# Optimization experiments

Measured on AMD Instinct MI355X. Metric: run time of the kernel, lower is better.

## Reference

```python
import jax, jax.numpy as jnp
import numpy as np

B, L, D_IN, D_H, D_OUT = 8, 1024, 1024, 1024, 1024


def setup_inputs() -> dict:
    key = jax.random.key(0)
    ks = jax.random.split(key, 9)
    s = 0.02  # weight scale to keep ReLU chain stable
    return {
        "leaves": jax.random.normal(ks[0], (B, L, D_IN), dtype=jnp.float32),
        "V_w": jax.random.normal(ks[1], (D_H, D_IN), dtype=jnp.float32) * s,
        "V_b": jax.random.normal(ks[2], (D_H,), dtype=jnp.float32) * s,
        "U_w": jax.random.normal(ks[3], (D_H, D_H), dtype=jnp.float32) * s,
        "U_b": jax.random.normal(ks[4], (D_H,), dtype=jnp.float32) * s,
        "W_w": jax.random.normal(ks[5], (D_H, D_H), dtype=jnp.float32) * s,
        "W_b": jax.random.normal(ks[6], (D_H,), dtype=jnp.float32) * s,
        "O_w": jax.random.normal(ks[7], (D_OUT, D_H), dtype=jnp.float32) * s,
        "O_b": jax.random.normal(ks[8], (D_OUT,), dtype=jnp.float32) * s,
    }


def reference(leaves, V_w, V_b, U_w, U_b, W_w, W_b, O_w, O_b):
    # Leaf encoding: h_leaf = relu(V(x))            [B, L, H]
    h = jax.nn.relu(jnp.einsum("bli,hi->blh", leaves, V_w) + V_b)
    # Depth-batched recursion over the complete binary tree:
    # combined = relu(U(left) + W(right)); log2(L) levels, node count halves.
    while h.shape[1] > 1:
        left, right = h[:, 0::2], h[:, 1::2]  # [B, n/2, H] each
        h = jax.nn.relu(
            jnp.einsum("bnh,gh->bng", left, U_w) + U_b
            + jnp.einsum("bnh,gh->bng", right, W_w) + W_b
        )
    root = h[:, 0]  # [B, H]
    logits = jnp.einsum("bh,oh->bo", root, O_w) + O_b
    return jax.nn.log_softmax(logits, axis=-1)
```

## Files before the change

### kernel.cpp

```cpp
#include <hip/hip_runtime.h>
#include <hip/hip_bf16.h>
#include <math.h>

typedef __bf16 bf16_t;
typedef __bf16 bf16x8 __attribute__((ext_vector_type(8)));
typedef __bf16 bf16x4 __attribute__((ext_vector_type(4)));
typedef float  f32x4  __attribute__((ext_vector_type(4)));

#define GLD_LDS16(g, l)                                                          \
  __builtin_amdgcn_global_load_lds((const __attribute__((address_space(1))) void*)(g), \
                                   (__attribute__((address_space(3))) void*)(l), 16, 0, 0)

__global__ __launch_bounds__(256) void k_cvt_all(const float* __restrict__ leaves,
                                                 const float* __restrict__ V_w,
                                                 const float* __restrict__ O_w,
                                                 const float* __restrict__ U_w,
                                                 const float* __restrict__ W_w,
                                                 const float* __restrict__ U_b,
                                                 const float* __restrict__ W_b,
                                                 bf16_t* __restrict__ leaves_bf,
                                                 bf16_t* __restrict__ Vw_bf,
                                                 bf16_t* __restrict__ Ow_bf,
                                                 bf16_t* __restrict__ UW_bf,
                                                 float* __restrict__ buw) {
  const int gtid = blockIdx.x * 256 + threadIdx.x;
  const int G = gridDim.x * 256;
  for (int i = gtid; i < 2097152; i += G) {
    float4 v = reinterpret_cast<const float4*>(leaves)[i];
    bf16x4 o; o[0] = (bf16_t)v.x; o[1] = (bf16_t)v.y; o[2] = (bf16_t)v.z; o[3] = (bf16_t)v.w;
    reinterpret_cast<bf16x4*>(leaves_bf)[i] = o;
  }
  for (int i = gtid; i < 262144; i += G) {
    float4 v = reinterpret_cast<const float4*>(V_w)[i];
    bf16x4 o; o[0] = (bf16_t)v.x; o[1] = (bf16_t)v.y; o[2] = (bf16_t)v.z; o[3] = (bf16_t)v.w;
    reinterpret_cast<bf16x4*>(Vw_bf)[i] = o;
  }
  for (int i = gtid; i < 262144; i += G) {
    float4 v = reinterpret_cast<const float4*>(O_w)[i];
    bf16x4 o; o[0] = (bf16_t)v.x; o[1] = (bf16_t)v.y; o[2] = (bf16_t)v.z; o[3] = (bf16_t)v.w;
    reinterpret_cast<bf16x4*>(Ow_bf)[i] = o;
  }
  for (int idx = gtid; idx < 524288; idx += G) {
    int i = idx * 4;
    int g = i >> 11;
    int k = i & 2047;
    const float* src = (k < 1024) ? (U_w + g * 1024 + k) : (W_w + g * 1024 + (k - 1024));
    float4 v = *reinterpret_cast<const float4*>(src);
    bf16x4 o; o[0] = (bf16_t)v.x; o[1] = (bf16_t)v.y; o[2] = (bf16_t)v.z; o[3] = (bf16_t)v.w;
    reinterpret_cast<bf16x4*>(UW_bf)[idx] = o;
  }
  if (gtid < 1024) buw[gtid] = U_b[gtid] + W_b[gtid];
}

template <int TM, int TN, bool SPLIT>
__global__ __launch_bounds__(256, (TM == 128 ? 3 : 4)) void k_gemm(
    const bf16_t* __restrict__ A, const bf16_t* __restrict__ Bw,
    const float* __restrict__ bias, bf16_t* __restrict__ C,
    float* __restrict__ P, int M, int Kstride, int kchunk) {
  constexpr int MI = TM / 32;
  constexpr int NJ = TN / 32;
  constexpr int VM = TM / 64 + TN / 64;
  __shared__ bf16_t As[3][TM * 32];
  __shared__ bf16_t Bs[3][TN * 32];

  const int tid = threadIdx.x;
  const int lane = tid & 63;
  const int wave = tid >> 6;
  const int wr = wave >> 1, wc = wave & 1;
  const int bm = blockIdx.x, bn = blockIdx.y, bz = blockIdx.z;

  const bf16_t* Abase = A + (size_t)bm * TM * Kstride + (size_t)bz * kchunk;
  const bf16_t* Bbase = Bw + (size_t)bn * TN * Kstride + (size_t)bz * kchunk;

  f32x4 acc[MI][NJ] = {};
  const int rl = lane & 15, kq = lane >> 4;

  auto stage = [&](int buf, int ko) {
#pragma unroll
    for (int it = 0; it < TM / 64; ++it) {
      int c = tid + 256 * it;
      int r = c >> 2, kbp = c & 3;
      int kb = kbp ^ ((r >> 1) & 3);
      GLD_LDS16(Abase + (size_t)r * Kstride + ko + kb * 8, &As[buf][c * 8]);
    }
#pragma unroll
    for (int it = 0; it < TN / 64; ++it) {
      int c = tid + 256 * it;
      int r = c >> 2, kbp = c & 3;
      int kb = kbp ^ ((r >> 1) & 3);
      GLD_LDS16(Bbase + (size_t)r * Kstride + ko + kb * 8, &Bs[buf][c * 8]);
    }
  };

  const int kiters = kchunk >> 5;
  stage(0, 0);
  stage(1, 32);

  int cur = 0;
  for (int t = 0; t < kiters; ++t) {
    if (t + 1 < kiters) asm volatile("s_waitcnt vmcnt(%0)" :: "i"(VM) : "memory");
    else                asm volatile("s_waitcnt vmcnt(0)" ::: "memory");
    __builtin_amdgcn_s_barrier();
    __builtin_amdgcn_sched_barrier(0);
    if (t + 2 < kiters) {
      int b2 = cur + 2; if (b2 >= 3) b2 -= 3;
      stage(b2, (t + 2) * 32);
    }
    bf16x8 af[MI], bfr[NJ];
#pragma unroll
    for (int i = 0; i < MI; ++i) {
      int r = wr * (TM / 2) + i * 16 + rl;
      int kbp = kq ^ ((r >> 1) & 3);
      af[i] = *reinterpret_cast<const bf16x8*>(&As[cur][r * 32 + kbp * 8]);
    }
#pragma unroll
    for (int j = 0; j < NJ; ++j) {
      int r = wc * (TN / 2) + j * 16 + rl;
      int kbp = kq ^ ((r >> 1) & 3);
      bfr[j] = *reinterpret_cast<const bf16x8*>(&Bs[cur][r * 32 + kbp * 8]);
    }
#pragma unroll
    for (int i = 0; i < MI; ++i)
#pragma unroll
      for (int j = 0; j < NJ; ++j)
        acc[i][j] = __builtin_amdgcn_mfma_f32_16x16x32_bf16(af[i], bfr[j], acc[i][j], 0, 0, 0);
    if (++cur >= 3) cur = 0;
  }

  const int rq = lane >> 4, cl = lane & 15;
  if (SPLIT) {
    float* Pp = P + (size_t)bz * M * 1024;
#pragma unroll
    for (int j = 0; j < NJ; ++j) {
      int gcol = bn * TN + wc * (TN / 2) + j * 16 + cl;
#pragma unroll
      for (int i = 0; i < MI; ++i) {
        int grow = bm * TM + wr * (TM / 2) + i * 16 + rq * 4;
#pragma unroll
        for (int reg = 0; reg < 4; ++reg)
          Pp[(size_t)(grow + reg) * 1024 + gcol] = acc[i][j][reg];
      }
    }
  } else {
#pragma unroll
    for (int j = 0; j < NJ; ++j) {
      int gcol = bn * TN + wc * (TN / 2) + j * 16 + cl;
      float bv = bias[gcol];
#pragma unroll
      for (int i = 0; i < MI; ++i) {
        int grow = bm * TM + wr * (TM / 2) + i * 16 + rq * 4;
#pragma unroll
        for (int reg = 0; reg < 4; ++reg) {
          float v = acc[i][j][reg] + bv;
          v = v > 0.0f ? v : 0.0f;
          C[(size_t)(grow + reg) * 1024 + gcol] = (bf16_t)v;
        }
      }
    }
  }
}

__global__ __launch_bounds__(256) void k_reduce(const float* __restrict__ P,
                                                const float* __restrict__ bias,
                                                bf16_t* __restrict__ C, int M, int ks) {
  constexpr int N = 1024;
  int idx = blockIdx.x * 256 + threadIdx.x;
  int col = (idx * 4) & (N - 1);
  int row = (idx * 4) >> 10;
  float4 s = *reinterpret_cast<const float4*>(P + (size_t)row * N + col);
  for (int z = 1; z < ks; ++z) {
    float4 v = *reinterpret_cast<const float4*>(P + ((size_t)z * M + row) * N + col);
    s.x += v.x; s.y += v.y; s.z += v.z; s.w += v.w;
  }
  float4 b = *reinterpret_cast<const float4*>(bias + col);
  bf16x4 o;
  o[0] = (bf16_t)fmaxf(s.x + b.x, 0.0f);
  o[1] = (bf16_t)fmaxf(s.y + b.y, 0.0f);
  o[2] = (bf16_t)fmaxf(s.z + b.z, 0.0f);
  o[3] = (bf16_t)fmaxf(s.w + b.w, 0.0f);
  reinterpret_cast<bf16x4*>(C)[idx] = o;
}

template <int KK, bool RELU, bool F32OUT>
__global__ __launch_bounds__(256) void k_tail(const bf16_t* __restrict__ A,
                                              const bf16_t* __restrict__ Bw,
                                              const float* __restrict__ bias,
                                              void* __restrict__ Cout, int M) {
  constexpr int N = 1024;
  constexpr int KPL = KK / 64;
  const int lane = threadIdx.x & 63;
  const int gw = blockIdx.x * 4 + (threadIdx.x >> 6);
  const int n = gw & (N - 1);
  const int mbase = (gw >> 10) * 8;
  const int k0 = lane * KPL;

  float bv[KPL];
  const bf16_t* bp = Bw + (size_t)n * KK + k0;
#pragma unroll
  for (int q = 0; q < KPL / 8; ++q) {
    bf16x8 v = *reinterpret_cast<const bf16x8*>(bp + q * 8);
#pragma unroll
    for (int j = 0; j < 8; ++j) bv[q * 8 + j] = (float)v[j];
  }

  float acc[8];
#pragma unroll
  for (int m = 0; m < 8; ++m) {
    const bf16_t* ap = A + (size_t)(mbase + m) * KK + k0;
    float s = 0.0f;
#pragma unroll
    for (int q = 0; q < KPL / 8; ++q) {
      bf16x8 v = *reinterpret_cast<const bf16x8*>(ap + q * 8);
#pragma unroll
      for (int j = 0; j < 8; ++j) s += (float)v[j] * bv[q * 8 + j];
    }
    acc[m] = s;
  }
#pragma unroll
  for (int m = 0; m < 8; ++m) {
#pragma unroll
    for (int off = 32; off >= 1; off >>= 1) acc[m] += __shfl_xor(acc[m], off, 64);
  }
  if (lane < 8 && mbase + lane < M) {
    float v = acc[lane] + bias[n];
    if (RELU) v = v > 0.0f ? v : 0.0f;
    if (F32OUT) ((float*)Cout)[(size_t)(mbase + lane) * N + n] = v;
    else        ((bf16_t*)Cout)[(size_t)(mbase + lane) * N + n] = (bf16_t)v;
  }
}

__global__ __launch_bounds__(256) void k_logsoftmax(const float* __restrict__ logits,
                                                    float* __restrict__ out) {
  int b = blockIdx.x;
  const float* x = logits + b * 1024;
  int tid = threadIdx.x;
  int wave = tid >> 6, lane = tid & 63;
  __shared__ float red[8];

  float m = -1e30f;
  for (int i = tid; i < 1024; i += 256) m = fmaxf(m, x[i]);
#pragma unroll
  for (int off = 32; off >= 1; off >>= 1) m = fmaxf(m, __shfl_xor(m, off, 64));
  if (lane == 0) red[wave] = m;
  __syncthreads();
  m = fmaxf(fmaxf(red[0], red[1]), fmaxf(red[2], red[3]));
  float s = 0.0f;
  for (int i = tid; i < 1024; i += 256) s += expf(x[i] - m);
#pragma unroll
  for (int off = 32; off >= 1; off >>= 1) s += __shfl_xor(s, off, 64);
  if (lane == 0) red[wave] = s;
  __syncthreads();
  float lse = m + logf(red[0] + red[1] + red[2] + red[3]);
  for (int i = tid; i < 1024; i += 256) out[b * 1024 + i] = x[i] - lse;
}

extern "C" void kernel_launch(void* const* d_in, const int* in_sizes, int n_in,
                              void* d_out, int out_size, void* d_ws, size_t ws_size,
                              hipStream_t stream) {
  const float* leaves = (const float*)d_in[0];
  const float* V_w = (const float*)d_in[1];
  const float* V_b = (const float*)d_in[2];
  const float* U_w = (const float*)d_in[3];
  const float* U_b = (const float*)d_in[4];
  const float* W_w = (const float*)d_in[5];
  const float* W_b = (const float*)d_in[6];
  const float* O_w = (const float*)d_in[7];
  const float* O_b = (const float*)d_in[8];
  float* out = (float*)d_out;

  char* ws = (char*)d_ws;
  size_t off = 0;
  auto alloc = [&](size_t bytes) -> void* {
    off = (off + 255) & ~(size_t)255;
    void* p = ws + off;
    off += bytes;
    return p;
  };

  const size_t MB16 = (size_t)8192 * 1024 * 2;
  bf16_t* leaves_bf = (bf16_t*)alloc(MB16);
  bf16_t* Vw_bf = (bf16_t*)alloc((size_t)1024 * 1024 * 2);
  bf16_t* UW_bf = (bf16_t*)alloc((size_t)2 * 1024 * 1024 * 2);
  bf16_t* Ow_bf = (bf16_t*)alloc((size_t)1024 * 1024 * 2);
  float* buw = (float*)alloc(1024 * 4);
  bf16_t* hA = (bf16_t*)alloc(MB16);
  float* logits = (float*)alloc(8 * 1024 * 4);
  float* Pbuf = (float*)alloc((size_t)2 * 4096 * 1024 * 4);
  (void)ws_size; (void)in_sizes; (void)n_in; (void)out_size;

  k_cvt_all<<<2048, 256, 0, stream>>>(leaves, V_w, O_w, U_w, W_w, U_b, W_b,
                                      leaves_bf, Vw_bf, Ow_bf, UW_bf, buw);

  k_gemm<128, 128, false><<<dim3(64, 8), 256, 0, stream>>>(
      leaves_bf, Vw_bf, V_b, hA, nullptr, 8192, 1024, 1024);

  bf16_t* src = hA;
  bf16_t* dst = leaves_bf;
  auto swap = [&]() { bf16_t* t = src; src = dst; dst = t; };

  k_gemm<128, 128, true><<<dim3(32, 8, 2), 256, 0, stream>>>(
      src, UW_bf, nullptr, nullptr, Pbuf, 4096, 2048, 1024);
  k_reduce<<<4096 * 1024 / 4 / 256, 256, 0, stream>>>(Pbuf, buw, dst, 4096, 2);
  swap();
  k_gemm<64, 128, true><<<dim3(32, 8, 2), 256, 0, stream>>>(
      src, UW_bf, nullptr, nullptr, Pbuf, 2048, 2048, 1024);
  k_reduce<<<2048 * 1024 / 4 / 256, 256, 0, stream>>>(Pbuf, buw, dst, 2048, 2);
  swap();
  k_gemm<64, 128, true><<<dim3(16, 8, 4), 256, 0, stream>>>(
      src, UW_bf, nullptr, nullptr, Pbuf, 1024, 2048, 512);
  k_reduce<<<1024 * 1024 / 4 / 256, 256, 0, stream>>>(Pbuf, buw, dst, 1024, 4);
  swap();
  k_gemm<64, 128, true><<<dim3(8, 8, 4), 256, 0, stream>>>(
      src, UW_bf, nullptr, nullptr, Pbuf, 512, 2048, 512);
  k_reduce<<<512 * 1024 / 4 / 256, 256, 0, stream>>>(Pbuf, buw, dst, 512, 4);
  swap();
  k_gemm<64, 128, true><<<dim3(4, 8, 8), 256, 0, stream>>>(
      src, UW_bf, nullptr, nullptr, Pbuf, 256, 2048, 256);
  k_reduce<<<256 * 1024 / 4 / 256, 256, 0, stream>>>(Pbuf, buw, dst, 256, 8);
  swap();
  k_gemm<64, 128, true><<<dim3(2, 8, 8), 256, 0, stream>>>(
      src, UW_bf, nullptr, nullptr, Pbuf, 128, 2048, 256);
  k_reduce<<<128 * 1024 / 4 / 256, 256, 0, stream>>>(Pbuf, buw, dst, 128, 8);
  swap();
  for (int M = 64; M >= 8; M >>= 1) {
    int blocks = (M / 8) * 1024 / 4;
    k_tail<2048, true, false><<<blocks, 256, 0, stream>>>(src, UW_bf, buw, dst, M);
    swap();
  }

  k_tail<1024, false, true><<<256, 256, 0, stream>>>(src, Ow_bf, O_b, logits, 8);
  k_logsoftmax<<<8, 256, 0, stream>>>(logits, out);
}
```

Baseline: 216.1 us.

## Deepen GEMM LDS pipeline to four stages and store split-K partials as bf16

The GEMM kernel goes from a 3-buffer to a 4-buffer LDS ring with three tiles prefetched ahead, and the vmcnt waits are adjusted to match. This hides more global-load latency, at the cost of more LDS per block and a lower occupancy hint in launch_bounds. Split-K partial sums are now written and read as bf16 instead of fp32, halving the partial-buffer traffic between the GEMM and the reduce kernel. That rounds each partial before summation, which costs some precision. The partial buffer allocation also grows in size.

```diff
diff --git a/kernel.cpp b/kernel.cpp
--- a/kernel.cpp
+++ b/kernel.cpp
@@ -53,15 +53,15 @@
 }
 
 template <int TM, int TN, bool SPLIT>
-__global__ __launch_bounds__(256, (TM == 128 ? 3 : 4)) void k_gemm(
+__global__ __launch_bounds__(256, (TM == 128 ? 2 : 3)) void k_gemm(
     const bf16_t* __restrict__ A, const bf16_t* __restrict__ Bw,
     const float* __restrict__ bias, bf16_t* __restrict__ C,
-    float* __restrict__ P, int M, int Kstride, int kchunk) {
+    bf16_t* __restrict__ P, int M, int Kstride, int kchunk) {
   constexpr int MI = TM / 32;
   constexpr int NJ = TN / 32;
   constexpr int VM = TM / 64 + TN / 64;
-  __shared__ bf16_t As[3][TM * 32];
-  __shared__ bf16_t Bs[3][TN * 32];
+  __shared__ bf16_t As[4][TM * 32];
+  __shared__ bf16_t Bs[4][TN * 32];
 
   const int tid = threadIdx.x;
   const int lane = tid & 63;
@@ -94,17 +94,20 @@
 
   const int kiters = kchunk >> 5;
   stage(0, 0);
-  stage(1, 32);
+  if (kiters > 1) stage(1, 32);
+  if (kiters > 2) stage(2, 64);
 
   int cur = 0;
   for (int t = 0; t < kiters; ++t) {
-    if (t + 1 < kiters) asm volatile("s_waitcnt vmcnt(%0)" :: "i"(VM) : "memory");
-    else                asm volatile("s_waitcnt vmcnt(0)" ::: "memory");
+    const int nin = kiters - 1 - t;
+    if (nin >= 2)      asm volatile("s_waitcnt vmcnt(%0)" :: "i"(2 * VM) : "memory");
+    else if (nin == 1) asm volatile("s_waitcnt vmcnt(%0)" :: "i"(VM) : "memory");
+    else               asm volatile("s_waitcnt vmcnt(0)" ::: "memory");
     __builtin_amdgcn_s_barrier();
     __builtin_amdgcn_sched_barrier(0);
-    if (t + 2 < kiters) {
-      int b2 = cur + 2; if (b2 >= 3) b2 -= 3;
-      stage(b2, (t + 2) * 32);
+    if (t + 3 < kiters) {
+      int b3 = cur + 3; if (b3 >= 4) b3 -= 4;
+      stage(b3, (t + 3) * 32);
     }
     bf16x8 af[MI], bfr[NJ];
 #pragma unroll
@@ -124,12 +127,12 @@
 #pragma unroll
       for (int j = 0; j < NJ; ++j)
         acc[i][j] = __builtin_amdgcn_mfma_f32_16x16x32_bf16(af[i], bfr[j], acc[i][j], 0, 0, 0);
-    if (++cur >= 3) cur = 0;
+    if (++cur >= 4) cur = 0;
   }
 
   const int rq = lane >> 4, cl = lane & 15;
   if (SPLIT) {
-    float* Pp = P + (size_t)bz * M * 1024;
+    bf16_t* Pp = P + (size_t)bz * M * 1024;
 #pragma unroll
     for (int j = 0; j < NJ; ++j) {
       int gcol = bn * TN + wc * (TN / 2) + j * 16 + cl;
@@ -138,7 +141,7 @@
         int grow = bm * TM + wr * (TM / 2) + i * 16 + rq * 4;
 #pragma unroll
         for (int reg = 0; reg < 4; ++reg)
-          Pp[(size_t)(grow + reg) * 1024 + gcol] = acc[i][j][reg];
+          Pp[(size_t)(grow + reg) * 1024 + gcol] = (bf16_t)acc[i][j][reg];
       }
     }
   } else {
@@ -160,24 +163,24 @@
   }
 }
 
-__global__ __launch_bounds__(256) void k_reduce(const float* __restrict__ P,
+__global__ __launch_bounds__(256) void k_reduce(const bf16_t* __restrict__ P,
                                                 const float* __restrict__ bias,
                                                 bf16_t* __restrict__ C, int M, int ks) {
   constexpr int N = 1024;
   int idx = blockIdx.x * 256 + threadIdx.x;
   int col = (idx * 4) & (N - 1);
   int row = (idx * 4) >> 10;
-  float4 s = *reinterpret_cast<const float4*>(P + (size_t)row * N + col);
-  for (int z = 1; z < ks; ++z) {
-    float4 v = *reinterpret_cast<const float4*>(P + ((size_t)z * M + row) * N + col);
-    s.x += v.x; s.y += v.y; s.z += v.z; s.w += v.w;
+  float s0 = 0.0f, s1 = 0.0f, s2 = 0.0f, s3 = 0.0f;
+  for (int z = 0; z < ks; ++z) {
+    bf16x4 v = *reinterpret_cast<const bf16x4*>(P + ((size_t)z * M + row) * N + col);
+    s0 += (float)v[0]; s1 += (float)v[1]; s2 += (float)v[2]; s3 += (float)v[3];
   }
   float4 b = *reinterpret_cast<const float4*>(bias + col);
   bf16x4 o;
-  o[0] = (bf16_t)fmaxf(s.x + b.x, 0.0f);
-  o[1] = (bf16_t)fmaxf(s.y + b.y, 0.0f);
-  o[2] = (bf16_t)fmaxf(s.z + b.z, 0.0f);
-  o[3] = (bf16_t)fmaxf(s.w + b.w, 0.0f);
+  o[0] = (bf16_t)fmaxf(s0 + b.x, 0.0f);
+  o[1] = (bf16_t)fmaxf(s1 + b.y, 0.0f);
+  o[2] = (bf16_t)fmaxf(s2 + b.z, 0.0f);
+  o[3] = (bf16_t)fmaxf(s3 + b.w, 0.0f);
   reinterpret_cast<bf16x4*>(C)[idx] = o;
 }
 
@@ -285,7 +288,7 @@
   float* buw = (float*)alloc(1024 * 4);
   bf16_t* hA = (bf16_t*)alloc(MB16);
   float* logits = (float*)alloc(8 * 1024 * 4);
-  float* Pbuf = (float*)alloc((size_t)2 * 4096 * 1024 * 4);
+  bf16_t* Pbuf = (bf16_t*)alloc((size_t)8 * 4096 * 1024 * 2);
   (void)ws_size; (void)in_sizes; (void)n_in; (void)out_size;
 
   k_cvt_all<<<2048, 256, 0, stream>>>(leaves, V_w, O_w, U_w, W_w, U_b, W_b,
```

Result: faster. 207.0 us (-4.2%).
